# Optimization experiments

Measured on AMD Instinct MI355X. Metric: run time of the kernel, lower is better.

Reference implementation:

```python
import jax, jax.numpy as jnp
import numpy as np

N = 50000          # nodes
E_RAND = 800000    # random edges (plus N self-loops)
IN, HID, OUT = 128, 32, 32
HEADS = (4, 4, 6)
NEG_SLOPE = 0.2    # DGL GATConv default leaky_relu slope


def setup_inputs() -> dict:
    key = jax.random.key(0)
    ks = jax.random.split(key, 16)
    s = 0.05
    x = jax.random.normal(ks[0], (N, IN), jnp.float32)
    # random graph + self loops (SELF_LOOP=True in the source)
    src = jnp.concatenate([jax.random.randint(ks[1], (E_RAND,), 0, N),
                           jnp.arange(N)]).astype(jnp.int32)
    dst = jnp.concatenate([jax.random.randint(ks[2], (E_RAND,), 0, N),
                           jnp.arange(N)]).astype(jnp.int32)
    H0, H1, H2 = HEADS
    return dict(
        x=x, src=src, dst=dst,
        W1=jax.random.normal(ks[3], (IN, H0 * HID), jnp.float32) * s,
        al1=jax.random.normal(ks[4], (H0, HID), jnp.float32) * s,
        ar1=jax.random.normal(ks[5], (H0, HID), jnp.float32) * s,
        b1=jnp.zeros((H0 * HID,), jnp.float32),
        W2=jax.random.normal(ks[6], (H0 * HID, H1 * HID), jnp.float32) * s,
        al2=jax.random.normal(ks[7], (H1, HID), jnp.float32) * s,
        ar2=jax.random.normal(ks[8], (H1, HID), jnp.float32) * s,
        b2=jnp.zeros((H1 * HID,), jnp.float32),
        W3=jax.random.normal(ks[9], (H1 * HID, H2 * OUT), jnp.float32) * s,
        al3=jax.random.normal(ks[10], (H2, OUT), jnp.float32) * s,
        ar3=jax.random.normal(ks[11], (H2, OUT), jnp.float32) * s,
        b3=jnp.zeros((H2 * OUT,), jnp.float32),
        resW3=jax.random.normal(ks[12], (H1 * HID, H2 * OUT), jnp.float32) * s,
    )


def gat_layer(h, src, dst, W, al, ar, b, residual=None, act_relu=True):
    """One DGL-style GATConv: fc -> per-edge leaky_relu attention -> edge
    softmax over incoming edges -> weighted scatter-sum -> (+res) + bias -> act."""
    n = h.shape[0]
    H, out = al.shape
    feat = (h @ W).reshape(n, H, out)                 # [N,H,out]
    el = jnp.sum(feat * al, axis=-1)                  # [N,H]
    er = jnp.sum(feat * ar, axis=-1)                  # [N,H]
    e = jax.nn.leaky_relu(el[src] + er[dst], NEG_SLOPE)  # [E,H]
    emax = jax.ops.segment_max(e, dst, num_segments=n)   # [N,H]
    ex = jnp.exp(e - emax[dst])                       # [E,H]
    denom = jax.ops.segment_sum(ex, dst, num_segments=n) # [N,H]
    alpha = ex / jnp.maximum(denom[dst], 1e-9)        # [E,H]
    msg = feat[src] * alpha[..., None]                # [E,H,out]
    rst = jax.ops.segment_sum(msg, dst, num_segments=n)  # [N,H,out]
    if residual is not None:
        rst = rst + residual
    rst = rst + b.reshape(1, H, out)
    return jax.nn.relu(rst) if act_relu else rst


def reference(x, src, dst, W1, al1, ar1, b1, W2, al2, ar2, b2,
              W3, al3, ar3, b3, resW3):
    n = x.shape[0]
    # layer 1: no residual, relu, flatten heads
    h1 = gat_layer(x, src, dst, W1, al1, ar1, b1).reshape(n, -1)
    # layer 2: residual is Identity (in_dim == heads*hid), relu, flatten
    res2 = h1.reshape(n, HEADS[1], HID)
    h2 = gat_layer(h1, src, dst, W2, al2, ar2, b2, residual=res2).reshape(n, -1)
    # layer 3: residual via linear projection (dims differ), no activation, mean heads
    res3 = (h2 @ resW3).reshape(n, HEADS[2], OUT)
    h3 = gat_layer(h2, src, dst, W3, al3, ar3, b3, residual=res3, act_relu=False)
    return h3.mean(axis=1)
```

## Files before the change

kernel.cpp:

```cpp
#include <hip/hip_runtime.h>
#include <math.h>


typedef _Float16 v8h __attribute__((ext_vector_type(8)));
typedef float f32x4 __attribute__((ext_vector_type(4)));

__device__ __host__ inline int pack_off(int n, int k) {
    return ((n >> 4) << 11) | ((k >> 5) << 9) | (((k >> 3) & 3) << 7) | ((n & 15) << 3) | (k & 7);
}


__global__ void hist_kernel(const int* __restrict__ dst, int E, int* __restrict__ deg) {
    int i = blockIdx.x * blockDim.x + threadIdx.x;
    if (i < E) atomicAdd(&deg[dst[i]], 1);
}


__global__ void scan_phaseA(const int* __restrict__ deg, int n, int* __restrict__ bsum) {
    __shared__ int red[4];
    int t = threadIdx.x;
    int base = blockIdx.x * 2048 + t * 8;
    int s = 0;
    #pragma unroll
    for (int q = 0; q < 8; q++) { int i = base + q; if (i < n) s += deg[i]; }
    #pragma unroll
    for (int off = 1; off < 64; off <<= 1) s += __shfl_xor(s, off);
    if ((t & 63) == 0) red[t >> 6] = s;
    __syncthreads();
    if (t == 0) bsum[blockIdx.x] = red[0] + red[1] + red[2] + red[3];
}

__global__ void scan_phaseB(int* __restrict__ bsum, int nb) {
    int lane = threadIdx.x & 63;
    int v = (lane < nb) ? bsum[lane] : 0;
    int inc = v;
    #pragma unroll
    for (int off = 1; off < 64; off <<= 1) {
        int u = __shfl_up(inc, off);
        if (lane >= off) inc += u;
    }
    int ex = inc - v;
    if (lane < nb) bsum[lane] = ex;
}

__global__ void scan_phaseC(const int* __restrict__ deg, int n, const int* __restrict__ bsum,
                            int* __restrict__ row_start, int E) {
    __shared__ int wsum[4];
    int t = threadIdx.x;
    int lane = t & 63, wv = t >> 6;
    int base = blockIdx.x * 2048 + t * 8;
    int v[8]; int s = 0;
    #pragma unroll
    for (int q = 0; q < 8; q++) { int i = base + q; v[q] = (i < n) ? deg[i] : 0; s += v[q]; }
    int inc = s;
    #pragma unroll
    for (int off = 1; off < 64; off <<= 1) {
        int u = __shfl_up(inc, off);
        if (lane >= off) inc += u;
    }
    if (lane == 63) wsum[wv] = inc;
    __syncthreads();
    int woff = 0;
    for (int w = 0; w < wv; w++) woff += wsum[w];
    int run = inc - s + woff + bsum[blockIdx.x];
    #pragma unroll
    for (int q = 0; q < 8; q++) {
        int i = base + q;
        if (i < n) row_start[i] = run;
        run += v[q];
    }
    if (blockIdx.x == 0 && t == 0) row_start[n] = E;
}

__global__ void fill_kernel(const int* __restrict__ src, const int* __restrict__ dst, int E,
                            const int* __restrict__ row_start, int* __restrict__ cursor,
                            int* __restrict__ csr_src) {
    int i = blockIdx.x * blockDim.x + threadIdx.x;
    if (i < E) {
        int d = dst[i];
        int pos = atomicAdd(&cursor[d], 1);
        csr_src[row_start[d] + pos] = src[i];
    }
}


__global__ void wsplit_all(const float* __restrict__ W1, const float* __restrict__ W2,
                           const float* __restrict__ W3, const float* __restrict__ Wr,
                           _Float16* __restrict__ o) {
    int i = blockIdx.x * blockDim.x + threadIdx.x;
    if (i >= 81920) return;
    float v; int ohi, e, stride;
    if (i < 16384) {
        e = i; int c = e >> 7, k = e & 127;
        v = W1[(size_t)k * 128 + c]; ohi = 0; stride = 16384;
    } else if (i < 32768) {
        e = i - 16384; int c = e >> 7, k = e & 127;
        v = W2[(size_t)k * 128 + c]; ohi = 32768; stride = 16384;
    } else {
        e = i - 32768; int c = e >> 7, k = e & 127;
        v = (c < 192) ? W3[(size_t)k * 192 + c] : Wr[(size_t)k * 192 + (c - 192)];
        ohi = 65536; stride = 49152;
    }
    int c = e >> 7, k = e & 127;
    int po = pack_off(c, k);
    _Float16 hv = (_Float16)v;
    o[ohi + po] = hv;
    o[ohi + stride + po] = (_Float16)(v - (float)hv);
}


__global__ void splitx_kernel(const float* __restrict__ x, _Float16* __restrict__ hi,
                              _Float16* __restrict__ lo, int N, int PT) {
    int i = blockIdx.x * blockDim.x + threadIdx.x;
    if (i >= PT * 2048) return;
    int mt = i >> 11, r = i & 2047;
    int q4 = r >> 9, quad = (r >> 7) & 3, ln = (r >> 3) & 15, j = r & 7;
    int n = mt * 16 + ln, k = q4 * 32 + quad * 8 + j;
    float v = (n < N) ? x[(size_t)n * 128 + k] : 0.f;
    _Float16 h = (_Float16)v;
    hi[i] = h;
    lo[i] = (_Float16)(v - (float)h);
}


template <int CC, int H>
__global__ __launch_bounds__(256, 4) void mfma_fc(
    const _Float16* __restrict__ Ahi, const _Float16* __restrict__ Alo,
    const _Float16* __restrict__ Bhi, const _Float16* __restrict__ Blo,
    const float* __restrict__ al, const float* __restrict__ ar,
    _Float16* __restrict__ feat_out,
    float* __restrict__ el, float* __restrict__ er, int N) {
    constexpr int TILES = CC / 16;
    int t = threadIdx.x;
    int wave = t >> 6, lane = t & 63;
    int ln = lane & 15, quad = lane >> 4;
    int mt = blockIdx.x * 4 + wave;

    f32x4 acc[TILES];
    #pragma unroll
    for (int i = 0; i < TILES; i++) acc[i] = (f32x4){0.f, 0.f, 0.f, 0.f};

    const _Float16* pa_h = Ahi + (size_t)mt * 2048 + lane * 8;
    const _Float16* pa_l = Alo + (size_t)mt * 2048 + lane * 8;

    #pragma unroll
    for (int q4 = 0; q4 < 4; q4++) {
        v8h ah = *(const v8h*)(pa_h + q4 * 512);
        v8h av = *(const v8h*)(pa_l + q4 * 512);
        #pragma unroll
        for (int tt = 0; tt < TILES; tt++) {
            size_t boff = (size_t)tt * 2048 + q4 * 512 + lane * 8;
            v8h bh = *(const v8h*)(Bhi + boff);
            v8h bl = *(const v8h*)(Blo + boff);
            acc[tt] = __builtin_amdgcn_mfma_f32_16x16x32_f16(av, bh, acc[tt], 0, 0, 0);
            acc[tt] = __builtin_amdgcn_mfma_f32_16x16x32_f16(ah, bl, acc[tt], 0, 0, 0);
            acc[tt] = __builtin_amdgcn_mfma_f32_16x16x32_f16(ah, bh, acc[tt], 0, 0, 0);
        }
    }

    #pragma unroll
    for (int tt = 0; tt < TILES; tt++) {
        int n = tt * 16 + ln;
        #pragma unroll
        for (int r = 0; r < 4; r++) {
            int m = mt * 16 + quad * 4 + r;
            if (m < N) feat_out[(size_t)m * CC + n] = (_Float16)acc[tt][r];
        }
    }
    #pragma unroll
    for (int hg = 0; hg < H; hg++) {
        float a0 = al[hg * 32 + ln], a1 = al[hg * 32 + 16 + ln];
        float r0 = ar[hg * 32 + ln], r1 = ar[hg * 32 + 16 + ln];
        #pragma unroll
        for (int r = 0; r < 4; r++) {
            float pl = acc[2 * hg][r] * a0 + acc[2 * hg + 1][r] * a1;
            float pr = acc[2 * hg][r] * r0 + acc[2 * hg + 1][r] * r1;
            #pragma unroll
            for (int off = 1; off < 16; off <<= 1) {
                pl += __shfl_xor(pl, off);
                pr += __shfl_xor(pr, off);
            }
            int m = mt * 16 + quad * 4 + r;
            if (ln == 0 && m < N) {
                el[(size_t)m * H + hg] = pl;
                er[(size_t)m * H + hg] = pr;
            }
        }
    }
}


__global__ __launch_bounds__(256, 3) void mfma_fc3(
    const _Float16* __restrict__ Ahi, const _Float16* __restrict__ Alo,
    const _Float16* __restrict__ B3h, const _Float16* __restrict__ B3l,
    const _Float16* __restrict__ Brh, const _Float16* __restrict__ Brl,
    const float* __restrict__ al, const float* __restrict__ ar,
    _Float16* __restrict__ feat_out, float* __restrict__ res_out,
    float* __restrict__ el, float* __restrict__ er, int N) {
    constexpr int CC = 192, H = 6, TILES = 12;
    const bool isres = (blockIdx.y == 1);
    const _Float16* __restrict__ Bhi = isres ? Brh : B3h;
    const _Float16* __restrict__ Blo = isres ? Brl : B3l;

    int t = threadIdx.x;
    int wave = t >> 6, lane = t & 63;
    int ln = lane & 15, quad = lane >> 4;
    int mt = blockIdx.x * 4 + wave;

    f32x4 acc[TILES];
    #pragma unroll
    for (int i = 0; i < TILES; i++) acc[i] = (f32x4){0.f, 0.f, 0.f, 0.f};

    const _Float16* pa_h = Ahi + (size_t)mt * 2048 + lane * 8;
    const _Float16* pa_l = Alo + (size_t)mt * 2048 + lane * 8;

    #pragma unroll
    for (int q4 = 0; q4 < 4; q4++) {
        v8h ah = *(const v8h*)(pa_h + q4 * 512);
        v8h av = *(const v8h*)(pa_l + q4 * 512);
        #pragma unroll
        for (int tt = 0; tt < TILES; tt++) {
            size_t boff = (size_t)tt * 2048 + q4 * 512 + lane * 8;
            v8h bh = *(const v8h*)(Bhi + boff);
            v8h bl = *(const v8h*)(Blo + boff);
            acc[tt] = __builtin_amdgcn_mfma_f32_16x16x32_f16(av, bh, acc[tt], 0, 0, 0);
            acc[tt] = __builtin_amdgcn_mfma_f32_16x16x32_f16(ah, bl, acc[tt], 0, 0, 0);
            acc[tt] = __builtin_amdgcn_mfma_f32_16x16x32_f16(ah, bh, acc[tt], 0, 0, 0);
        }
    }

    if (!isres) {
        #pragma unroll
        for (int tt = 0; tt < TILES; tt++) {
            int n = tt * 16 + ln;
            #pragma unroll
            for (int r = 0; r < 4; r++) {
                int m = mt * 16 + quad * 4 + r;
                if (m < N) feat_out[(size_t)m * CC + n] = (_Float16)acc[tt][r];
            }
        }
        #pragma unroll
        for (int hg = 0; hg < H; hg++) {
            float a0 = al[hg * 32 + ln], a1 = al[hg * 32 + 16 + ln];
            float r0 = ar[hg * 32 + ln], r1 = ar[hg * 32 + 16 + ln];
            #pragma unroll
            for (int r = 0; r < 4; r++) {
                float pl = acc[2 * hg][r] * a0 + acc[2 * hg + 1][r] * a1;
                float pr = acc[2 * hg][r] * r0 + acc[2 * hg + 1][r] * r1;
                #pragma unroll
                for (int off = 1; off < 16; off <<= 1) {
                    pl += __shfl_xor(pl, off);
                    pr += __shfl_xor(pr, off);
                }
                int m = mt * 16 + quad * 4 + r;
                if (ln == 0 && m < N) {
                    el[(size_t)m * H + hg] = pl;
                    er[(size_t)m * H + hg] = pr;
                }
            }
        }
    } else {
        #pragma unroll
        for (int tt = 0; tt < TILES; tt++) {
            int n = tt * 16 + ln;
            #pragma unroll
            for (int r = 0; r < 4; r++) {
                int m = mt * 16 + quad * 4 + r;
                if (m < N) res_out[(size_t)m * CC + n] = acc[tt][r];
            }
        }
    }
}


template <int H, bool RELU, bool MEAN, int RES, bool PACK>
__global__ __launch_bounds__(256) void gat_agg_wave(
        const _Float16* __restrict__ feat, const float* __restrict__ el,
        const float* __restrict__ er, const int* __restrict__ row_start,
        const int* __restrict__ csr_src, const float* __restrict__ bias,
        const float* __restrict__ res_plain,
        const _Float16* __restrict__ res_hi, const _Float16* __restrict__ res_lo,
        float* __restrict__ out, _Float16* __restrict__ out_hi, _Float16* __restrict__ out_lo,
        int N) {
    constexpr int ROW = H * 32;
    constexpr int LPG = ROW / 8;
    constexpr int G   = 64 / LPG;
    int wv = threadIdx.x >> 6, lane = threadIdx.x & 63;
    int n = blockIdx.x * 4 + wv;
    if (n >= N) return;

    int d8 = lane % LPG;
    int g  = lane / LPG;
    int hd = d8 >> 2;

    int start = row_start[n], end = row_start[n + 1];
    float er_hd = er[(size_t)n * H + hd];
    const _Float16* fbase = feat + 8 * d8;

    float acc[8];
    #pragma unroll
    for (int q = 0; q < 8; q++) acc[q] = 0.f;
    float wsum = 0.f;

    int j = (g < G) ? (start + g) : end;
    for (; j + G < end; j += 2 * G) {
        int s0 = csr_src[j];
        int s1 = csr_src[j + G];
        float e0 = el[(size_t)s0 * H + hd] + er_hd;
        float e1 = el[(size_t)s1 * H + hd] + er_hd;
        e0 = (e0 >= 0.f) ? e0 : 0.2f * e0;
        e1 = (e1 >= 0.f) ? e1 : 0.2f * e1;
        float w0 = __expf(e0);
        float w1 = __expf(e1);
        v8h v0 = *(const v8h*)(fbase + (size_t)s0 * ROW);
        v8h v1 = *(const v8h*)(fbase + (size_t)s1 * ROW);
        wsum += w0 + w1;
        #pragma unroll
        for (int q = 0; q < 8; q++) acc[q] += w0 * (float)v0[q] + w1 * (float)v1[q];
    }
    if (j < end) {
        int s0 = csr_src[j];
        float e0 = el[(size_t)s0 * H + hd] + er_hd;
        e0 = (e0 >= 0.f) ? e0 : 0.2f * e0;
        float w0 = __expf(e0);
        v8h v0 = *(const v8h*)(fbase + (size_t)s0 * ROW);
        wsum += w0;
        #pragma unroll
        for (int q = 0; q < 8; q++) acc[q] += w0 * (float)v0[q];
    }

    if constexpr (G == 4) {
        #pragma unroll
        for (int q = 0; q < 8; q++) {
            acc[q] += __shfl_xor(acc[q], 16);
            acc[q] += __shfl_xor(acc[q], 32);
        }
        wsum += __shfl_xor(wsum, 16);
        wsum += __shfl_xor(wsum, 32);
    } else {
        #pragma unroll
        for (int q = 0; q < 8; q++) acc[q] += __shfl(acc[q], lane + 24);
        wsum += __shfl(wsum, lane + 24);
    }

    float inv = 1.0f / fmaxf(wsum, 1e-9f);
    float4 bv0 = *(const float4*)(bias + 8 * d8);
    float4 bv1 = *(const float4*)(bias + 8 * d8 + 4);
    float r[8];
    r[0] = acc[0] * inv + bv0.x; r[1] = acc[1] * inv + bv0.y;
    r[2] = acc[2] * inv + bv0.z; r[3] = acc[3] * inv + bv0.w;
    r[4] = acc[4] * inv + bv1.x; r[5] = acc[5] * inv + bv1.y;
    r[6] = acc[6] * inv + bv1.z; r[7] = acc[7] * inv + bv1.w;

    if constexpr (RES == 1) {
        int off = pack_off(n, 8 * d8);
        v8h rh = *(const v8h*)(res_hi + off);
        v8h rl = *(const v8h*)(res_lo + off);
        #pragma unroll
        for (int q = 0; q < 8; q++) r[q] += (float)rh[q] + (float)rl[q];
    } else if constexpr (RES == 2) {
        float4 rv0 = *(const float4*)(res_plain + (size_t)n * ROW + 8 * d8);
        float4 rv1 = *(const float4*)(res_plain + (size_t)n * ROW + 8 * d8 + 4);
        r[0] += rv0.x; r[1] += rv0.y; r[2] += rv0.z; r[3] += rv0.w;
        r[4] += rv1.x; r[5] += rv1.y; r[6] += rv1.z; r[7] += rv1.w;
    }
    if constexpr (RELU) {
        #pragma unroll
        for (int q = 0; q < 8; q++) r[q] = fmaxf(r[q], 0.f);
    }

    if constexpr (PACK) {
        if (lane < LPG) {
            int off = pack_off(n, 8 * d8);
            v8h hh, ll;
            #pragma unroll
            for (int q = 0; q < 8; q++) {
                hh[q] = (_Float16)r[q];
                ll[q] = (_Float16)(r[q] - (float)hh[q]);
            }
            *(v8h*)(out_hi + off) = hh;
            *(v8h*)(out_lo + off) = ll;
        }
    } else if constexpr (MEAN) {
        int qb = d8 & 3;
        float s[8];
        #pragma unroll
        for (int q = 0; q < 8; q++) {
            s[q] = r[q];
            #pragma unroll
            for (int hh2 = 1; hh2 < H; hh2++) s[q] += __shfl(r[q], qb + 4 * hh2);
        }
        if (lane < 4) {
            const float sc = 1.0f / H;
            *(float4*)(out + (size_t)n * 32 + 8 * lane) =
                make_float4(s[0] * sc, s[1] * sc, s[2] * sc, s[3] * sc);
            *(float4*)(out + (size_t)n * 32 + 8 * lane + 4) =
                make_float4(s[4] * sc, s[5] * sc, s[6] * sc, s[7] * sc);
        }
    } else {
        if (lane < LPG) {
            *(float4*)(out + (size_t)n * ROW + 8 * d8) = make_float4(r[0], r[1], r[2], r[3]);
            *(float4*)(out + (size_t)n * ROW + 8 * d8 + 4) = make_float4(r[4], r[5], r[6], r[7]);
        }
    }
}


extern "C" void kernel_launch(void* const* d_in, const int* in_sizes, int n_in,
                              void* d_out, int out_size, void* d_ws, size_t ws_size,
                              hipStream_t stream) {
    const float* x    = (const float*)d_in[0];
    const int*   src  = (const int*)d_in[1];
    const int*   dst  = (const int*)d_in[2];
    const float* W1   = (const float*)d_in[3];
    const float* al1  = (const float*)d_in[4];
    const float* ar1  = (const float*)d_in[5];
    const float* b1   = (const float*)d_in[6];
    const float* W2   = (const float*)d_in[7];
    const float* al2  = (const float*)d_in[8];
    const float* ar2  = (const float*)d_in[9];
    const float* b2   = (const float*)d_in[10];
    const float* W3   = (const float*)d_in[11];
    const float* al3  = (const float*)d_in[12];
    const float* ar3  = (const float*)d_in[13];
    const float* b3   = (const float*)d_in[14];
    const float* resW3= (const float*)d_in[15];
    float* out = (float*)d_out;

    const int N = in_sizes[0] / 128;
    const int E = in_sizes[1];
    const int TILES16 = (N + 15) / 16;
    const int PT = (TILES16 + 3) & ~3;
    const int NB = PT / 4;
    const int NSB = (N + 2047) / 2048;

    float* fws  = (float*)d_ws;
    float* res3 = fws;
    float* elb  = res3 + (size_t)N * 192;
    float* erb  = elb + (size_t)N * 6;
    _Float16* feat_h = (_Float16*)(erb + (size_t)N * 6);
    _Float16* xh_hi  = feat_h + (size_t)N * 192;
    _Float16* xh_lo  = xh_hi + (size_t)PT * 2048;
    _Float16* h1_hi  = xh_lo + (size_t)PT * 2048;
    _Float16* h1_lo  = h1_hi + (size_t)PT * 2048;
    _Float16* wts    = h1_lo + (size_t)PT * 2048;
    int* deg       = (int*)(wts + 163840);
    int* row_start = deg + N;
    int* bsum      = row_start + (N + 1);
    int* csr_src   = bsum + 64;

    const _Float16* W1h = wts;
    const _Float16* W1l = wts + 16384;
    const _Float16* W2h = wts + 32768;
    const _Float16* W2l = wts + 49152;
    const _Float16* W3h = wts + 65536;
    const _Float16* W3l = wts + 65536 + 49152;
    const _Float16* Wrh = W3h + 192 * 128;
    const _Float16* Wrl = W3l + 192 * 128;

    hipMemsetAsync(deg, 0, (size_t)N * sizeof(int), stream);
    hist_kernel<<<dim3((E + 255) / 256), dim3(256), 0, stream>>>(dst, E, deg);
    scan_phaseA<<<dim3(NSB), dim3(256), 0, stream>>>(deg, N, bsum);
    scan_phaseB<<<dim3(1), dim3(64), 0, stream>>>(bsum, NSB);
    scan_phaseC<<<dim3(NSB), dim3(256), 0, stream>>>(deg, N, bsum, row_start, E);
    hipMemsetAsync(deg, 0, (size_t)N * sizeof(int), stream);
    fill_kernel<<<dim3((E + 255) / 256), dim3(256), 0, stream>>>(src, dst, E, row_start, deg, csr_src);
    wsplit_all<<<dim3(320), dim3(256), 0, stream>>>(W1, W2, W3, resW3, wts);
    splitx_kernel<<<dim3((PT * 2048 + 255) / 256), dim3(256), 0, stream>>>(x, xh_hi, xh_lo, N, PT);

    dim3 ab((N + 3) / 4);

    mfma_fc<128, 4><<<dim3(NB), dim3(256), 0, stream>>>(
        xh_hi, xh_lo, W1h, W1l, al1, ar1, feat_h, elb, erb, N);
    gat_agg_wave<4, true, false, 0, true><<<ab, dim3(256), 0, stream>>>(
        feat_h, elb, erb, row_start, csr_src, b1,
        nullptr, nullptr, nullptr, nullptr, h1_hi, h1_lo, N);

    mfma_fc<128, 4><<<dim3(NB), dim3(256), 0, stream>>>(
        h1_hi, h1_lo, W2h, W2l, al2, ar2, feat_h, elb, erb, N);
    gat_agg_wave<4, true, false, 1, true><<<ab, dim3(256), 0, stream>>>(
        feat_h, elb, erb, row_start, csr_src, b2,
        nullptr, h1_hi, h1_lo, nullptr, xh_hi, xh_lo, N);

    mfma_fc3<<<dim3(NB, 2), dim3(256), 0, stream>>>(
        xh_hi, xh_lo, W3h, W3l, Wrh, Wrl, al3, ar3, feat_h, res3, elb, erb, N);
    gat_agg_wave<6, false, true, 2, false><<<ab, dim3(256), 0, stream>>>(
        feat_h, elb, erb, row_start, csr_src, b3,
        res3, nullptr, nullptr, out, nullptr, nullptr, N);
}
```

Before: 424.5 us.

## Pre-average residual weights, store layer features head-planar, aggregate per head

The layer-3 residual projection is folded algebraically: since the output is a head mean, resW3 is averaged over heads into a 32-column weight. This lets the layer-3 GEMM compute 224 columns in one pass instead of a second 192-column residual grid, and only a 32-wide residual buffer is written. Layers 1-2 now store features as per-head planes. A new per-head aggregation kernel, with blocks swizzled by head, reads compact 64-byte rows so gathers can hit cache better. In exchange, the aggregation launches H times more blocks, and each one rereads the CSR and el.

New measurement: 508.2 us. 1.2x slower.

```diff
diff --git a/kernel.cpp b/kernel.cpp
--- a/kernel.cpp
+++ b/kernel.cpp
@@ -14,7 +14,6 @@
     int i = blockIdx.x * blockDim.x + threadIdx.x;
     if (i < E) atomicAdd(&deg[dst[i]], 1);
 }
-
 
 __global__ void scan_phaseA(const int* __restrict__ deg, int n, int* __restrict__ bsum) {
     __shared__ int red[4];
@@ -88,21 +87,25 @@
                            const float* __restrict__ W3, const float* __restrict__ Wr,
                            _Float16* __restrict__ o) {
     int i = blockIdx.x * blockDim.x + threadIdx.x;
-    if (i >= 81920) return;
-    float v; int ohi, e, stride;
+    if (i >= 61440) return;
+    float v; int ohi, stride, po;
     if (i < 16384) {
-        e = i; int c = e >> 7, k = e & 127;
-        v = W1[(size_t)k * 128 + c]; ohi = 0; stride = 16384;
+        int e = i, c = e >> 7, k = e & 127;
+        v = W1[(size_t)k * 128 + c]; ohi = 0; stride = 16384; po = pack_off(c, k);
     } else if (i < 32768) {
-        e = i - 16384; int c = e >> 7, k = e & 127;
-        v = W2[(size_t)k * 128 + c]; ohi = 32768; stride = 16384;
+        int e = i - 16384, c = e >> 7, k = e & 127;
+        v = W2[(size_t)k * 128 + c]; ohi = 32768; stride = 16384; po = pack_off(c, k);
+    } else if (i < 57344) {
+        int e = i - 32768, c = e >> 7, k = e & 127;
+        v = W3[(size_t)k * 192 + c]; ohi = 65536; stride = 28672; po = pack_off(c, k);
     } else {
-        e = i - 32768; int c = e >> 7, k = e & 127;
-        v = (c < 192) ? W3[(size_t)k * 192 + c] : Wr[(size_t)k * 192 + (c - 192)];
-        ohi = 65536; stride = 49152;
-    }
-    int c = e >> 7, k = e & 127;
-    int po = pack_off(c, k);
+        int e = i - 57344, c = e >> 7, k = e & 127;
+        float s = 0.f;
+        #pragma unroll
+        for (int h = 0; h < 6; h++) s += Wr[(size_t)k * 192 + h * 32 + c];
+        v = s * (1.0f / 6.0f);
+        ohi = 65536; stride = 28672; po = 24576 + pack_off(c, k);
+    }
     _Float16 hv = (_Float16)v;
     o[ohi + po] = hv;
     o[ohi + stride + po] = (_Float16)(v - (float)hv);
@@ -161,10 +164,12 @@
     #pragma unroll
     for (int tt = 0; tt < TILES; tt++) {
         int n = tt * 16 + ln;
+        int head = n >> 5, wi = n & 31;
+        _Float16* fo = feat_out + (size_t)head * N * 32;
         #pragma unroll
         for (int r = 0; r < 4; r++) {
             int m = mt * 16 + quad * 4 + r;
-            if (m < N) feat_out[(size_t)m * CC + n] = (_Float16)acc[tt][r];
+            if (m < N) fo[(size_t)m * 32 + wi] = (_Float16)acc[tt][r];
         }
     }
     #pragma unroll
@@ -192,16 +197,11 @@
 
 __global__ __launch_bounds__(256, 3) void mfma_fc3(
     const _Float16* __restrict__ Ahi, const _Float16* __restrict__ Alo,
-    const _Float16* __restrict__ B3h, const _Float16* __restrict__ B3l,
-    const _Float16* __restrict__ Brh, const _Float16* __restrict__ Brl,
+    const _Float16* __restrict__ Bhi, const _Float16* __restrict__ Blo,
     const float* __restrict__ al, const float* __restrict__ ar,
-    _Float16* __restrict__ feat_out, float* __restrict__ res_out,
+    _Float16* __restrict__ feat_out, float* __restrict__ res_m,
     float* __restrict__ el, float* __restrict__ er, int N) {
-    constexpr int CC = 192, H = 6, TILES = 12;
-    const bool isres = (blockIdx.y == 1);
-    const _Float16* __restrict__ Bhi = isres ? Brh : B3h;
-    const _Float16* __restrict__ Blo = isres ? Brl : B3l;
-
+    constexpr int CC = 192, H = 6, TILES = 14;
     int t = threadIdx.x;
     int wave = t >> 6, lane = t & 63;
     int ln = lane & 15, quad = lane >> 4;
@@ -229,62 +229,133 @@
         }
     }
 
-    if (!isres) {
-        #pragma unroll
-        for (int tt = 0; tt < TILES; tt++) {
-            int n = tt * 16 + ln;
+    #pragma unroll
+    for (int tt = 0; tt < 12; tt++) {
+        int n = tt * 16 + ln;
+        #pragma unroll
+        for (int r = 0; r < 4; r++) {
+            int m = mt * 16 + quad * 4 + r;
+            if (m < N) feat_out[(size_t)m * CC + n] = (_Float16)acc[tt][r];
+        }
+    }
+    #pragma unroll
+    for (int tt = 12; tt < 14; tt++) {
+        int n32 = (tt - 12) * 16 + ln;
+        #pragma unroll
+        for (int r = 0; r < 4; r++) {
+            int m = mt * 16 + quad * 4 + r;
+            if (m < N) res_m[(size_t)m * 32 + n32] = acc[tt][r];
+        }
+    }
+    #pragma unroll
+    for (int hg = 0; hg < H; hg++) {
+        float a0 = al[hg * 32 + ln], a1 = al[hg * 32 + 16 + ln];
+        float r0 = ar[hg * 32 + ln], r1 = ar[hg * 32 + 16 + ln];
+        #pragma unroll
+        for (int r = 0; r < 4; r++) {
+            float pl = acc[2 * hg][r] * a0 + acc[2 * hg + 1][r] * a1;
+            float pr = acc[2 * hg][r] * r0 + acc[2 * hg + 1][r] * r1;
             #pragma unroll
-            for (int r = 0; r < 4; r++) {
-                int m = mt * 16 + quad * 4 + r;
-                if (m < N) feat_out[(size_t)m * CC + n] = (_Float16)acc[tt][r];
+            for (int off = 1; off < 16; off <<= 1) {
+                pl += __shfl_xor(pl, off);
+                pr += __shfl_xor(pr, off);
             }
-        }
-        #pragma unroll
-        for (int hg = 0; hg < H; hg++) {
-            float a0 = al[hg * 32 + ln], a1 = al[hg * 32 + 16 + ln];
-            float r0 = ar[hg * 32 + ln], r1 = ar[hg * 32 + 16 + ln];
-            #pragma unroll
-            for (int r = 0; r < 4; r++) {
-                float pl = acc[2 * hg][r] * a0 + acc[2 * hg + 1][r] * a1;
-                float pr = acc[2 * hg][r] * r0 + acc[2 * hg + 1][r] * r1;
-                #pragma unroll
-                for (int off = 1; off < 16; off <<= 1) {
-                    pl += __shfl_xor(pl, off);
-                    pr += __shfl_xor(pr, off);
-                }
-                int m = mt * 16 + quad * 4 + r;
-                if (ln == 0 && m < N) {
-                    el[(size_t)m * H + hg] = pl;
-                    er[(size_t)m * H + hg] = pr;
-                }
+            int m = mt * 16 + quad * 4 + r;
+            if (ln == 0 && m < N) {
+                el[(size_t)m * H + hg] = pl;
+                er[(size_t)m * H + hg] = pr;
             }
         }
-    } else {
-        #pragma unroll
-        for (int tt = 0; tt < TILES; tt++) {
-            int n = tt * 16 + ln;
-            #pragma unroll
-            for (int r = 0; r < 4; r++) {
-                int m = mt * 16 + quad * 4 + r;
-                if (m < N) res_out[(size_t)m * CC + n] = acc[tt][r];
-            }
-        }
-    }
-}
-
-
-template <int H, bool RELU, bool MEAN, int RES, bool PACK>
-__global__ __launch_bounds__(256) void gat_agg_wave(
+    }
+}
+
+
+template <int H, int RES>
+__global__ __launch_bounds__(256) void gat_agg_head(
+        const _Float16* __restrict__ feat_planes, const float* __restrict__ el,
+        const float* __restrict__ er, const int* __restrict__ row_start,
+        const int* __restrict__ csr_src, const float* __restrict__ bias,
+        const _Float16* __restrict__ res_hi, const _Float16* __restrict__ res_lo,
+        _Float16* __restrict__ out_hi, _Float16* __restrict__ out_lo,
+        int N, int NG8) {
+    unsigned b = blockIdx.x;
+    unsigned C = (unsigned)(NG8 * H) >> 3;
+    unsigned t = (b & 7u) * C + (b >> 3);
+    int h = (int)(t / (unsigned)NG8);
+    int ng = (int)(t - (unsigned)h * (unsigned)NG8);
+    int wv = threadIdx.x >> 6, lane = threadIdx.x & 63;
+    int n = ng * 4 + wv;
+    if (n >= N) return;
+
+    int q = lane & 3;
+    int g = lane >> 2;
+
+    int start = row_start[n], end = row_start[n + 1];
+    float er_h = er[(size_t)n * H + h];
+    const _Float16* fbase = feat_planes + (size_t)h * N * 32 + q * 8;
+
+    float acc[8];
+    #pragma unroll
+    for (int i = 0; i < 8; i++) acc[i] = 0.f;
+    float wsum = 0.f;
+
+    for (int j = start + g; j < end; j += 16) {
+        int s0 = csr_src[j];
+        float e0 = el[(size_t)s0 * H + h] + er_h;
+        e0 = (e0 >= 0.f) ? e0 : 0.2f * e0;
+        float w0 = __expf(e0);
+        v8h v0 = *(const v8h*)(fbase + (size_t)s0 * 32);
+        wsum += w0;
+        #pragma unroll
+        for (int i = 0; i < 8; i++) acc[i] += w0 * (float)v0[i];
+    }
+
+    #pragma unroll
+    for (int off = 4; off < 64; off <<= 1) {
+        #pragma unroll
+        for (int i = 0; i < 8; i++) acc[i] += __shfl_xor(acc[i], off);
+        wsum += __shfl_xor(wsum, off);
+    }
+
+    float inv = 1.0f / fmaxf(wsum, 1e-9f);
+    float4 bv0 = *(const float4*)(bias + h * 32 + q * 8);
+    float4 bv1 = *(const float4*)(bias + h * 32 + q * 8 + 4);
+    float r[8];
+    r[0] = acc[0] * inv + bv0.x; r[1] = acc[1] * inv + bv0.y;
+    r[2] = acc[2] * inv + bv0.z; r[3] = acc[3] * inv + bv0.w;
+    r[4] = acc[4] * inv + bv1.x; r[5] = acc[5] * inv + bv1.y;
+    r[6] = acc[6] * inv + bv1.z; r[7] = acc[7] * inv + bv1.w;
+
+    if constexpr (RES == 1) {
+        int off = pack_off(n, h * 32 + q * 8);
+        v8h rh = *(const v8h*)(res_hi + off);
+        v8h rl = *(const v8h*)(res_lo + off);
+        #pragma unroll
+        for (int i = 0; i < 8; i++) r[i] += (float)rh[i] + (float)rl[i];
+    }
+    #pragma unroll
+    for (int i = 0; i < 8; i++) r[i] = fmaxf(r[i], 0.f);
+
+    if (lane < 4) {
+        int po = pack_off(n, h * 32 + lane * 8);
+        v8h hh, ll;
+        #pragma unroll
+        for (int i = 0; i < 8; i++) {
+            hh[i] = (_Float16)r[i];
+            ll[i] = (_Float16)(r[i] - (float)hh[i]);
+        }
+        *(v8h*)(out_hi + po) = hh;
+        *(v8h*)(out_lo + po) = ll;
+    }
+}
+
+
+__global__ __launch_bounds__(256) void gat_agg_mean6(
         const _Float16* __restrict__ feat, const float* __restrict__ el,
         const float* __restrict__ er, const int* __restrict__ row_start,
         const int* __restrict__ csr_src, const float* __restrict__ bias,
-        const float* __restrict__ res_plain,
-        const _Float16* __restrict__ res_hi, const _Float16* __restrict__ res_lo,
-        float* __restrict__ out, _Float16* __restrict__ out_hi, _Float16* __restrict__ out_lo,
-        int N) {
-    constexpr int ROW = H * 32;
-    constexpr int LPG = ROW / 8;
-    constexpr int G   = 64 / LPG;
+        const float* __restrict__ res_m, float* __restrict__ out, int N) {
+    constexpr int H = 6, ROW = 192, LPG = 24, G = 2;
     int wv = threadIdx.x >> 6, lane = threadIdx.x & 63;
     int n = blockIdx.x * 4 + wv;
     if (n >= N) return;
@@ -329,19 +400,9 @@
         for (int q = 0; q < 8; q++) acc[q] += w0 * (float)v0[q];
     }
 
-    if constexpr (G == 4) {
-        #pragma unroll
-        for (int q = 0; q < 8; q++) {
-            acc[q] += __shfl_xor(acc[q], 16);
-            acc[q] += __shfl_xor(acc[q], 32);
-        }
-        wsum += __shfl_xor(wsum, 16);
-        wsum += __shfl_xor(wsum, 32);
-    } else {
-        #pragma unroll
-        for (int q = 0; q < 8; q++) acc[q] += __shfl(acc[q], lane + 24);
-        wsum += __shfl(wsum, lane + 24);
-    }
+    #pragma unroll
+    for (int q = 0; q < 8; q++) acc[q] += __shfl(acc[q], lane + 24);
+    wsum += __shfl(wsum, lane + 24);
 
     float inv = 1.0f / fmaxf(wsum, 1e-9f);
     float4 bv0 = *(const float4*)(bias + 8 * d8);
@@ -352,56 +413,24 @@
     r[4] = acc[4] * inv + bv1.x; r[5] = acc[5] * inv + bv1.y;
     r[6] = acc[6] * inv + bv1.z; r[7] = acc[7] * inv + bv1.w;
 
-    if constexpr (RES == 1) {
-        int off = pack_off(n, 8 * d8);
-        v8h rh = *(const v8h*)(res_hi + off);
-        v8h rl = *(const v8h*)(res_lo + off);
-        #pragma unroll
-        for (int q = 0; q < 8; q++) r[q] += (float)rh[q] + (float)rl[q];
-    } else if constexpr (RES == 2) {
-        float4 rv0 = *(const float4*)(res_plain + (size_t)n * ROW + 8 * d8);
-        float4 rv1 = *(const float4*)(res_plain + (size_t)n * ROW + 8 * d8 + 4);
-        r[0] += rv0.x; r[1] += rv0.y; r[2] += rv0.z; r[3] += rv0.w;
-        r[4] += rv1.x; r[5] += rv1.y; r[6] += rv1.z; r[7] += rv1.w;
-    }
-    if constexpr (RELU) {
-        #pragma unroll
-        for (int q = 0; q < 8; q++) r[q] = fmaxf(r[q], 0.f);
-    }
-
-    if constexpr (PACK) {
-        if (lane < LPG) {
-            int off = pack_off(n, 8 * d8);
-            v8h hh, ll;
-            #pragma unroll
-            for (int q = 0; q < 8; q++) {
-                hh[q] = (_Float16)r[q];
-                ll[q] = (_Float16)(r[q] - (float)hh[q]);
-            }
-            *(v8h*)(out_hi + off) = hh;
-            *(v8h*)(out_lo + off) = ll;
-        }
-    } else if constexpr (MEAN) {
-        int qb = d8 & 3;
-        float s[8];
-        #pragma unroll
-        for (int q = 0; q < 8; q++) {
-            s[q] = r[q];
-            #pragma unroll
-            for (int hh2 = 1; hh2 < H; hh2++) s[q] += __shfl(r[q], qb + 4 * hh2);
-        }
-        if (lane < 4) {
-            const float sc = 1.0f / H;
-            *(float4*)(out + (size_t)n * 32 + 8 * lane) =
-                make_float4(s[0] * sc, s[1] * sc, s[2] * sc, s[3] * sc);
-            *(float4*)(out + (size_t)n * 32 + 8 * lane + 4) =
-                make_float4(s[4] * sc, s[5] * sc, s[6] * sc, s[7] * sc);
-        }
-    } else {
-        if (lane < LPG) {
-            *(float4*)(out + (size_t)n * ROW + 8 * d8) = make_float4(r[0], r[1], r[2], r[3]);
-            *(float4*)(out + (size_t)n * ROW + 8 * d8 + 4) = make_float4(r[4], r[5], r[6], r[7]);
-        }
+    int qb = d8 & 3;
+    float s[8];
+    #pragma unroll
+    for (int q = 0; q < 8; q++) {
+        s[q] = r[q];
+        #pragma unroll
+        for (int hh2 = 1; hh2 < H; hh2++) s[q] += __shfl(r[q], qb + 4 * hh2);
+    }
+    if (lane < 4) {
+        const float sc = 1.0f / 6.0f;
+        float4 rm0 = *(const float4*)(res_m + (size_t)n * 32 + 8 * lane);
+        float4 rm1 = *(const float4*)(res_m + (size_t)n * 32 + 8 * lane + 4);
+        *(float4*)(out + (size_t)n * 32 + 8 * lane) =
+            make_float4(s[0] * sc + rm0.x, s[1] * sc + rm0.y,
+                        s[2] * sc + rm0.z, s[3] * sc + rm0.w);
+        *(float4*)(out + (size_t)n * 32 + 8 * lane + 4) =
+            make_float4(s[4] * sc + rm1.x, s[5] * sc + rm1.y,
+                        s[6] * sc + rm1.z, s[7] * sc + rm1.w);
     }
 }
 
@@ -433,10 +462,12 @@
     const int PT = (TILES16 + 3) & ~3;
     const int NB = PT / 4;
     const int NSB = (N + 2047) / 2048;
+    const int NG = (N + 3) / 4;
+    const int NG8 = (NG + 1) & ~1;
 
     float* fws  = (float*)d_ws;
-    float* res3 = fws;
-    float* elb  = res3 + (size_t)N * 192;
+    float* res_m = fws;
+    float* elb  = res_m + (size_t)N * 32;
     float* erb  = elb + (size_t)N * 6;
     _Float16* feat_h = (_Float16*)(erb + (size_t)N * 6);
     _Float16* xh_hi  = feat_h + (size_t)N * 192;
@@ -444,7 +475,7 @@
     _Float16* h1_hi  = xh_lo + (size_t)PT * 2048;
     _Float16* h1_lo  = h1_hi + (size_t)PT * 2048;
     _Float16* wts    = h1_lo + (size_t)PT * 2048;
-    int* deg       = (int*)(wts + 163840);
+    int* deg       = (int*)(wts + 122880);
     int* row_start = deg + N;
     int* bsum      = row_start + (N + 1);
     int* csr_src   = bsum + 64;
@@ -453,10 +484,8 @@
     const _Float16* W1l = wts + 16384;
     const _Float16* W2h = wts + 32768;
     const _Float16* W2l = wts + 49152;
-    const _Float16* W3h = wts + 65536;
-    const _Float16* W3l = wts + 65536 + 49152;
-    const _Float16* Wrh = W3h + 192 * 128;
-    const _Float16* Wrl = W3l + 192 * 128;
+    const _Float16* B3h = wts + 65536;
+    const _Float16* B3l = wts + 94208;
 
     hipMemsetAsync(deg, 0, (size_t)N * sizeof(int), stream);
     hist_kernel<<<dim3((E + 255) / 256), dim3(256), 0, stream>>>(dst, E, deg);
@@ -465,26 +494,23 @@
     scan_phaseC<<<dim3(NSB), dim3(256), 0, stream>>>(deg, N, bsum, row_start, E);
     hipMemsetAsync(deg, 0, (size_t)N * sizeof(int), stream);
     fill_kernel<<<dim3((E + 255) / 256), dim3(256), 0, stream>>>(src, dst, E, row_start, deg, csr_src);
-    wsplit_all<<<dim3(320), dim3(256), 0, stream>>>(W1, W2, W3, resW3, wts);
+    wsplit_all<<<dim3(240), dim3(256), 0, stream>>>(W1, W2, W3, resW3, wts);
     splitx_kernel<<<dim3((PT * 2048 + 255) / 256), dim3(256), 0, stream>>>(x, xh_hi, xh_lo, N, PT);
-
-    dim3 ab((N + 3) / 4);
 
     mfma_fc<128, 4><<<dim3(NB), dim3(256), 0, stream>>>(
         xh_hi, xh_lo, W1h, W1l, al1, ar1, feat_h, elb, erb, N);
-    gat_agg_wave<4, true, false, 0, true><<<ab, dim3(256), 0, stream>>>(
+    gat_agg_head<4, 0><<<dim3(NG8 * 4), dim3(256), 0, stream>>>(
         feat_h, elb, erb, row_start, csr_src, b1,
-        nullptr, nullptr, nullptr, nullptr, h1_hi, h1_lo, N);
+        nullptr, nullptr, h1_hi, h1_lo, N, NG8);
 
     mfma_fc<128, 4><<<dim3(NB), dim3(256), 0, stream>>>(
         h1_hi, h1_lo, W2h, W2l, al2, ar2, feat_h, elb, erb, N);
-    gat_agg_wave<4, true, false, 1, true><<<ab, dim3(256), 0, stream>>>(
+    gat_agg_head<4, 1><<<dim3(NG8 * 4), dim3(256), 0, stream>>>(
         feat_h, elb, erb, row_start, csr_src, b2,
-        nullptr, h1_hi, h1_lo, nullptr, xh_hi, xh_lo, N);
-
-    mfma_fc3<<<dim3(NB, 2), dim3(256), 0, stream>>>(
-        xh_hi, xh_lo, W3h, W3l, Wrh, Wrl, al3, ar3, feat_h, res3, elb, erb, N);
-    gat_agg_wave<6, false, true, 2, false><<<ab, dim3(256), 0, stream>>>(
-        feat_h, elb, erb, row_start, csr_src, b3,
-        res3, nullptr, nullptr, out, nullptr, nullptr, N);
-}
+        h1_hi, h1_lo, xh_hi, xh_lo, N, NG8);
+
+    mfma_fc3<<<dim3(NB), dim3(256), 0, stream>>>(
+        xh_hi, xh_lo, B3h, B3l, al3, ar3, feat_h, res_m, elb, erb, N);
+    gat_agg_mean6<<<dim3((N + 3) / 4), dim3(256), 0, stream>>>(
+        feat_h, elb, erb, row_start, csr_src, b3, res_m, out, N);
+}
```
